# Optimization experiments

Hardware: AMD Instinct MI355X
Metric: run time of the kernel (lower is better)

## Reference

```python
import jax, jax.numpy as jnp
import numpy as np
import math


def _conv1x1(x, w, b):
    # x: [B,C,H,W], w: [O,C], b: [O] -> [B,O,H,W]
    return jnp.einsum('oc,bchw->bohw', w, x) + b[None, :, None, None]


def _attn_branch(x, f_w, f_b, g_w, g_b, h_w, h_b, gamma):
    B, C, H, W = x.shape
    N = H * W
    k_dim = C // 8
    f = _conv1x1(x, f_w, f_b).reshape(B, k_dim, N)  # [B,k,N]
    g = _conv1x1(x, g_w, g_b).reshape(B, k_dim, N)  # [B,k,N]
    # attention[b, n, m] = sum_k f[b,k,n] * g[b,k,m] / sqrt(k_dim)
    scores = jnp.einsum('bkn,bkm->bnm', f, g) / math.sqrt(k_dim)
    attn = jax.nn.softmax(scores, axis=2)  # softmax over last dim (dim=2)
    h = _conv1x1(x, h_w, h_b).reshape(B, C, N)  # [B,C,N]
    sa_map = jnp.einsum('bcn,bnm->bcm', h, attn).reshape(B, C, H, W)
    return gamma[0] * sa_map + x


def setup_inputs() -> dict:
    key = jax.random.key(0)
    ks = jax.random.split(key, 8)
    B, C, H, W = 4, 256, 64, 64
    kd = C // 8
    scale_in = 1.0 / math.sqrt(C)
    return {
        'x1': jax.random.normal(ks[0], (B, C, H, W), jnp.float32),
        'x2': jax.random.normal(ks[1], (B, C, H, W), jnp.float32),
        'f_w': jax.random.normal(ks[2], (kd, C), jnp.float32) * scale_in,
        'f_b': jnp.zeros((kd,), jnp.float32),
        'g_w': jax.random.normal(ks[3], (kd, C), jnp.float32) * scale_in,
        'g_b': jnp.zeros((kd,), jnp.float32),
        'h1_w': jax.random.normal(ks[4], (C, C), jnp.float32) * scale_in,
        'h1_b': jnp.zeros((C,), jnp.float32),
        'h2_w': jax.random.normal(ks[5], (C, C), jnp.float32) * scale_in,
        'h2_b': jnp.zeros((C,), jnp.float32),
        'gamma1': jax.random.normal(ks[6], (1,), jnp.float32),
        'gamma2': jax.random.normal(ks[7], (1,), jnp.float32),
    }


def reference(x1, x2, f_w, f_b, g_w, g_b, h1_w, h1_b, h2_w, h2_b, gamma1, gamma2):
    y1 = _attn_branch(x1, f_w, f_b, g_w, g_b, h1_w, h1_b, gamma1)
    y2 = _attn_branch(x2, f_w, f_b, g_w, g_b, h2_w, h2_b, gamma2)
    return (y1, y2)
```

## Files before the change

### kernel.cpp

```cpp
#include <hip/hip_runtime.h>
#include <hip/hip_bf16.h>
#include <math.h>

#define NDIM 4096
#define CDIM 256
#define KD   32
#define SCALE 0.17677669529663687f
#define SHIFT 8.0f

typedef __attribute__((ext_vector_type(8))) short short8;
typedef __attribute__((ext_vector_type(4))) float f32x4;
typedef unsigned short u16;
typedef unsigned int u32;

__device__ __forceinline__ u32 f2bf(float x) {
  union { float f; u32 u; } v; v.f = x;
  return (v.u + 0x7FFFu + ((v.u >> 16) & 1u)) >> 16;
}

__device__ __forceinline__ u32 pack_bf16x2(float a, float b) {
  __hip_bfloat162 h2 = __float22bfloat162_rn(make_float2(a, b));
  u32 r;
  __builtin_memcpy(&r, &h2, 4);
  return r;
}

#define MFMA16(a, b, c) __builtin_amdgcn_mfma_f32_16x16x32_bf16((a), (b), (c), 0, 0, 0)

__global__ void cast_all_kernel(const float* __restrict__ h1w,
                                const float* __restrict__ h2w,
                                const float* __restrict__ fw,
                                const float* __restrict__ gw,
                                u16* __restrict__ dst) {
  int i = blockIdx.x * 256 + threadIdx.x;
  float v;
  if (i < 65536) v = h1w[i];
  else if (i < 131072) v = h2w[i - 65536];
  else if (i < 139264) v = fw[i - 131072];
  else v = gw[i - 139264];
  dst[i] = (u16)f2bf(v);
}

__global__ __launch_bounds__(256) void transpose_cast_kernel(
    const float* __restrict__ x1, const float* __restrict__ x2,
    u16* __restrict__ xt) {
  __shared__ float ts[64][68];
  const int t = threadIdx.x;
  const int ntile = blockIdx.x * 64, Ctile = blockIdx.y * 64, z = blockIdx.z;
  const float* xb = ((z >> 2) ? x2 : x1) + (size_t)(z & 3) * CDIM * NDIM;
  u16* xtb = xt + (size_t)z * NDIM * CDIM;
  const int r = t >> 4, c4 = (t & 15) * 4;
#pragma unroll
  for (int i = 0; i < 4; i++) {
    float4 v = *(const float4*)&xb[(size_t)(Ctile + r + i * 16) * NDIM + ntile + c4];
    *(float4*)&ts[r + i * 16][c4] = v;
  }
  __syncthreads();
  const int n = t >> 2, Cg = (t & 3) * 16;
  u32 pk[8];
#pragma unroll
  for (int j = 0; j < 8; j++) {
    u32 lo = f2bf(ts[Cg + 2 * j][n]);
    u32 hi = f2bf(ts[Cg + 2 * j + 1][n]);
    pk[j] = lo | (hi << 16);
  }
  uint4* dst = (uint4*)&xtb[(size_t)(ntile + n) * CDIM + Ctile + Cg];
  dst[0] = make_uint4(pk[0], pk[1], pk[2], pk[3]);
  dst[1] = make_uint4(pk[4], pk[5], pk[6], pk[7]);
}

__global__ __launch_bounds__(256) void conv_fg_kernel(
    const u16* __restrict__ Wf, const float* __restrict__ fbias,
    const u16* __restrict__ Wg, const float* __restrict__ gbias,
    const u16* __restrict__ xt, u16* __restrict__ ftT, u16* __restrict__ gtT) {
  const int t = threadIdx.x, w = t >> 6, l = t & 63, li = l & 15, q = l >> 4;
  const int ntile = blockIdx.x * 64, bb = blockIdx.y;
  const u16* xtb = xt + (size_t)bb * NDIM * CDIM;
  f32x4 zero4 = {0.f, 0.f, 0.f, 0.f};
  f32x4 acc[2][2];
  for (int i = 0; i < 2; i++) for (int j = 0; j < 2; j++) acc[i][j] = zero4;
  const int nrow = ntile + w * 16 + li;

  for (int k0 = 0; k0 < CDIM; k0 += 32) {
    short8 bx = *(const short8*)&xtb[(size_t)nrow * CDIM + k0 + q * 8];
    short8 af0 = *(const short8*)&Wf[(size_t)(li) * CDIM + k0 + q * 8];
    short8 af1 = *(const short8*)&Wf[(size_t)(16 + li) * CDIM + k0 + q * 8];
    short8 ag0 = *(const short8*)&Wg[(size_t)(li) * CDIM + k0 + q * 8];
    short8 ag1 = *(const short8*)&Wg[(size_t)(16 + li) * CDIM + k0 + q * 8];
    acc[0][0] = MFMA16(af0, bx, acc[0][0]);
    acc[0][1] = MFMA16(af1, bx, acc[0][1]);
    acc[1][0] = MFMA16(ag0, bx, acc[1][0]);
    acc[1][1] = MFMA16(ag1, bx, acc[1][1]);
  }
  u16* outs[2] = {ftT + (size_t)bb * NDIM * KD, gtT + (size_t)bb * NDIM * KD};
  const float* biases[2] = {fbias, gbias};
#pragma unroll
  for (int fg = 0; fg < 2; fg++) {
#pragma unroll
    for (int os = 0; os < 2; os++) {
      float b0 = biases[fg][os * 16 + q * 4 + 0];
      float b1 = biases[fg][os * 16 + q * 4 + 1];
      float b2 = biases[fg][os * 16 + q * 4 + 2];
      float b3 = biases[fg][os * 16 + q * 4 + 3];
      u32 p0 = f2bf(acc[fg][os][0] + b0) | (f2bf(acc[fg][os][1] + b1) << 16);
      u32 p1 = f2bf(acc[fg][os][2] + b2) | (f2bf(acc[fg][os][3] + b3) << 16);
      *(uint2*)&outs[fg][(size_t)nrow * KD + os * 16 + q * 4] = make_uint2(p0, p1);
    }
  }
}

__global__ __launch_bounds__(256) void stats_kernel(
    const u16* __restrict__ ft, const u16* __restrict__ gt,
    float* __restrict__ L) {
  __shared__ float zred[32][64];
  const int t = threadIdx.x, w = t >> 6, l = t & 63, li = l & 15, q = l >> 4;
  const int n0 = blockIdx.x * 32;
  const int bb = blockIdx.z * 4 + blockIdx.y;
  const u16* ftb = ft + (size_t)bb * NDIM * KD;
  const u16* gtb = gt + (size_t)bb * NDIM * KD;
  f32x4 zero4 = {0.f, 0.f, 0.f, 0.f};

  short8 a0 = *(const short8*)&ftb[(size_t)(n0 + li) * KD + q * 8];
  short8 a1 = *(const short8*)&ftb[(size_t)(n0 + 16 + li) * KD + q * 8];
  f32x4 z0 = zero4, z1 = zero4;

#pragma unroll 2
  for (int it = 0; it < 64; it++) {
    int m = (it * 4 + w) * 16;
    short8 bf = *(const short8*)&gtb[(size_t)(m + li) * KD + q * 8];
    f32x4 S0 = MFMA16(a0, bf, zero4);
    f32x4 S1 = MFMA16(a1, bf, zero4);
#pragma unroll
    for (int reg = 0; reg < 4; reg++) {
      z0[reg] += __expf(S0[reg] * SCALE - SHIFT);
      z1[reg] += __expf(S1[reg] * SCALE - SHIFT);
    }
  }
#pragma unroll
  for (int reg = 0; reg < 4; reg++) {
    zred[q * 4 + reg][w * 16 + li] = z0[reg];
    zred[16 + q * 4 + reg][w * 16 + li] = z1[reg];
  }
  __syncthreads();
  const int r = t >> 3, i8 = t & 7;
  float4 s1 = *(const float4*)&zred[r][i8 * 8];
  float4 s2 = *(const float4*)&zred[r][i8 * 8 + 4];
  float sum = s1.x + s1.y + s1.z + s1.w + s2.x + s2.y + s2.z + s2.w;
  sum += __shfl_xor(sum, 1, 8);
  sum += __shfl_xor(sum, 2, 8);
  sum += __shfl_xor(sum, 4, 8);
  if (i8 == 0) L[(size_t)bb * NDIM + n0 + r] = SHIFT + __logf(sum);
}

__global__ __launch_bounds__(256) void conv_h_kernel(
    const u16* __restrict__ Wall, const float* __restrict__ b1,
    const float* __restrict__ b2, const u16* __restrict__ xt,
    const float* __restrict__ L, u16* __restrict__ outH) {
  const int t = threadIdx.x, w = t >> 6, l = t & 63, li = l & 15, q = l >> 4;
  const int ntile = blockIdx.x * 64;
  const int o0 = blockIdx.y * 64 + w * 16;
  const int bb = blockIdx.z, branch = bb >> 2;
  const u16* W = Wall + (size_t)branch * CDIM * CDIM;
  const float* bias = branch ? b2 : b1;
  const u16* xtb = xt + (size_t)bb * NDIM * CDIM;
  const float* Lb = L + (size_t)bb * NDIM;
  u16* ob = outH + (size_t)bb * CDIM * NDIM;
  f32x4 zero4 = {0.f, 0.f, 0.f, 0.f};
  f32x4 acc[4];
  for (int i = 0; i < 4; i++) acc[i] = zero4;

  for (int k0 = 0; k0 < CDIM; k0 += 32) {
    short8 a = *(const short8*)&W[(size_t)(o0 + li) * CDIM + k0 + q * 8];
#pragma unroll
    for (int ns = 0; ns < 4; ns++) {
      short8 bf = *(const short8*)&xtb[(size_t)(ntile + ns * 16 + li) * CDIM + k0 + q * 8];
      acc[ns] = MFMA16(a, bf, acc[ns]);
    }
  }
  float bv[4];
#pragma unroll
  for (int reg = 0; reg < 4; reg++) bv[reg] = bias[o0 + q * 4 + reg];
#pragma unroll
  for (int ns = 0; ns < 4; ns++) {
    int n = ntile + ns * 16 + li;
    float ex = __expf(-Lb[n]);
#pragma unroll
    for (int reg = 0; reg < 4; reg++) {
      int c = o0 + q * 4 + reg;
      ob[(size_t)c * NDIM + n] = (u16)f2bf((acc[ns][reg] + bv[reg]) * ex);
    }
  }
}

__global__ __launch_bounds__(1024, 4) void apply_kernel(
    const u16* __restrict__ ft, const u16* __restrict__ gt,
    const u16* __restrict__ h,
    const float* __restrict__ x1, const float* __restrict__ x2,
    const float* __restrict__ gamma1, const float* __restrict__ gamma2,
    float* __restrict__ out) {
  __shared__ u16 Pt[2][128][132];
  const int t = threadIdx.x, w = t >> 6, l = t & 63, li = l & 15, q = l >> 4;
  const int bid = blockIdx.x;
  const int bb = bid & 7;
  const int mtile = (bid >> 3) * 128;
  const int br = bb >> 2, b = bb & 3;
  const u16* ftb = ft + (size_t)bb * NDIM * KD;
  const u16* gtb = gt + (size_t)bb * NDIM * KD;
  const u16* hb = h + (size_t)bb * CDIM * NDIM;
  const float* xb = (br ? x2 : x1) + (size_t)b * CDIM * NDIM;
  const float gmv = br ? gamma2[0] : gamma1[0];
  float* ob = out + (size_t)bb * CDIM * NDIM;

  const int msub_s = w >> 1, npair = w & 1;
  const int c0 = (w & 7) * 32;
  const int mg = (w >> 3) * 64;
  f32x4 zero4 = {0.f, 0.f, 0.f, 0.f};
  short8 gfrag = *(const short8*)&gtb[(size_t)(mtile + msub_s * 16 + li) * KD + q * 8];

  f32x4 acc[2][4];
  for (int i = 0; i < 2; i++) for (int j = 0; j < 4; j++) acc[i][j] = zero4;

  u32 Ppk[4][2];
  short8 afA[4];

#pragma unroll
  for (int j = 0; j < 4; j++) {
    int n = npair * 64 + j * 16;
    short8 a = *(const short8*)&ftb[(size_t)(n + li) * KD + q * 8];
    f32x4 S = MFMA16(a, gfrag, zero4);
    Ppk[j][0] = pack_bf16x2(__expf(S[0] * SCALE), __expf(S[1] * SCALE));
    Ppk[j][1] = pack_bf16x2(__expf(S[2] * SCALE), __expf(S[3] * SCALE));
  }
#pragma unroll
  for (int j = 0; j < 4; j++)
    afA[j] = *(const short8*)&ftb[(size_t)(128 + npair * 64 + j * 16 + li) * KD + q * 8];

  for (int i = 0; i < 32; i++) {
    const int n0 = i * 128;
    const int buf = i & 1;
    short8 ah[2][4];
#pragma unroll
    for (int cs = 0; cs < 2; cs++)
#pragma unroll
      for (int kh = 0; kh < 4; kh++)
        ah[cs][kh] = *(const short8*)
            &hb[(size_t)(c0 + cs * 16 + li) * NDIM + n0 + kh * 32 + q * 8];

#pragma unroll
    for (int j = 0; j < 4; j++)
      *(uint2*)&Pt[buf][msub_s * 16 + li][npair * 64 + j * 16 + q * 4] =
          make_uint2(Ppk[j][0], Ppk[j][1]);

#pragma unroll
    for (int j = 0; j < 4; j++) {
      f32x4 S = MFMA16(afA[j], gfrag, zero4);
      Ppk[j][0] = pack_bf16x2(__expf(S[0] * SCALE), __expf(S[1] * SCALE));
      Ppk[j][1] = pack_bf16x2(__expf(S[2] * SCALE), __expf(S[3] * SCALE));
    }

    asm volatile("s_waitcnt lgkmcnt(0)" ::: "memory");
    __builtin_amdgcn_s_barrier();

    {
      int ch2 = (i + 2 < 32) ? i + 2 : 31;
#pragma unroll
      for (int j = 0; j < 4; j++)
        afA[j] = *(const short8*)
            &ftb[(size_t)(ch2 * 128 + npair * 64 + j * 16 + li) * KD + q * 8];
    }

#pragma unroll
    for (int kh = 0; kh < 4; kh++) {
#pragma unroll
      for (int ms = 0; ms < 4; ms++) {
        short8 bm = *(const short8*)&Pt[buf][mg + ms * 16 + li][kh * 32 + q * 8];
        acc[0][ms] = MFMA16(ah[0][kh], bm, acc[0][ms]);
        acc[1][ms] = MFMA16(ah[1][kh], bm, acc[1][ms]);
      }
    }
  }

#pragma unroll
  for (int cs = 0; cs < 2; cs++) {
#pragma unroll
    for (int ms = 0; ms < 4; ms++) {
#pragma unroll
      for (int reg = 0; reg < 4; reg++) {
        int c = c0 + cs * 16 + q * 4 + reg;
        int m = mtile + mg + ms * 16 + li;
        size_t idx = (size_t)c * NDIM + m;
        ob[idx] = gmv * acc[cs][ms][reg] + xb[idx];
      }
    }
  }
}

extern "C" void kernel_launch(void* const* d_in, const int* in_sizes, int n_in,
                              void* d_out, int out_size, void* d_ws, size_t ws_size,
                              hipStream_t stream) {
  const float* x1 = (const float*)d_in[0];
  const float* x2 = (const float*)d_in[1];
  const float* f_w = (const float*)d_in[2];
  const float* f_b = (const float*)d_in[3];
  const float* g_w = (const float*)d_in[4];
  const float* g_b = (const float*)d_in[5];
  const float* h1_w = (const float*)d_in[6];
  const float* h1_b = (const float*)d_in[7];
  const float* h2_w = (const float*)d_in[8];
  const float* h2_b = (const float*)d_in[9];
  const float* gamma1 = (const float*)d_in[10];
  const float* gamma2 = (const float*)d_in[11];
  float* out = (float*)d_out;

  char* ws = (char*)d_ws;
  u16* xt  = (u16*)(ws);
  u16* wh  = (u16*)(ws + 16777216);
  u16* ftw = (u16*)(ws + 33554432);
  u16* gtw = (u16*)(ws + 35651584);
  u16* wWh = (u16*)(ws + 37748736);
  u16* wWf = (u16*)(ws + 38010880);
  u16* wWg = (u16*)(ws + 38027264);
  float* Lw = (float*)(ws + 38043648);

  cast_all_kernel<<<576, 256, 0, stream>>>(h1_w, h2_w, f_w, g_w, wWh);

  transpose_cast_kernel<<<dim3(64, 4, 8), 256, 0, stream>>>(x1, x2, xt);

  conv_fg_kernel<<<dim3(64, 8), 256, 0, stream>>>(wWf, f_b, wWg, g_b, xt, ftw, gtw);

  stats_kernel<<<dim3(128, 4, 2), 256, 0, stream>>>(ftw, gtw, Lw);

  conv_h_kernel<<<dim3(64, 4, 8), 256, 0, stream>>>(wWh, h1_b, h2_b, xt, Lw, wh);

  apply_kernel<<<256, 1024, 0, stream>>>(ftw, gtw, wh, x1, x2,
                                         gamma1, gamma2, out);
}
```

Before: 336.8 us.

## Split attention kernel into producer/consumer warp-specialized wavefronts

Even wavefronts now compute the softmax numerator tile (f·g MFMA plus exp) into a double-buffered LDS tile, and odd wavefronts consume the previous tile with h in a PV MFMA loop. The consumer raises its scheduling priority, and its h loads are double-buffered per k-chunk. The consumer operands are swapped so the epilogue can write float4 vectorized output. The aim is to overlap the exp/score work with the matmul, at the cost of half the waves doing MFMA accumulation and more accumulator registers per consumer wave.

```diff
diff --git a/kernel.cpp b/kernel.cpp
--- a/kernel.cpp
+++ b/kernel.cpp
@@ -211,85 +211,83 @@
   const float gmv = br ? gamma2[0] : gamma1[0];
   float* ob = out + (size_t)bb * CDIM * NDIM;
 
-  const int msub_s = w >> 1, npair = w & 1;
-  const int c0 = (w & 7) * 32;
-  const int mg = (w >> 3) * 64;
+  const bool producer = (w & 1) == 0;
+  const int pidx = w >> 1;
+  const int c0 = (w >> 1) * 32;
   f32x4 zero4 = {0.f, 0.f, 0.f, 0.f};
-  short8 gfrag = *(const short8*)&gtb[(size_t)(mtile + msub_s * 16 + li) * KD + q * 8];
-
-  f32x4 acc[2][4];
-  for (int i = 0; i < 2; i++) for (int j = 0; j < 4; j++) acc[i][j] = zero4;
-
-  u32 Ppk[4][2];
-  short8 afA[4];
-
-#pragma unroll
-  for (int j = 0; j < 4; j++) {
-    int n = npair * 64 + j * 16;
-    short8 a = *(const short8*)&ftb[(size_t)(n + li) * KD + q * 8];
-    f32x4 S = MFMA16(a, gfrag, zero4);
-    Ppk[j][0] = pack_bf16x2(__expf(S[0] * SCALE), __expf(S[1] * SCALE));
-    Ppk[j][1] = pack_bf16x2(__expf(S[2] * SCALE), __expf(S[3] * SCALE));
-  }
-#pragma unroll
-  for (int j = 0; j < 4; j++)
-    afA[j] = *(const short8*)&ftb[(size_t)(128 + npair * 64 + j * 16 + li) * KD + q * 8];
-
-  for (int i = 0; i < 32; i++) {
-    const int n0 = i * 128;
-    const int buf = i & 1;
-    short8 ah[2][4];
-#pragma unroll
-    for (int cs = 0; cs < 2; cs++)
-#pragma unroll
-      for (int kh = 0; kh < 4; kh++)
-        ah[cs][kh] = *(const short8*)
-            &hb[(size_t)(c0 + cs * 16 + li) * NDIM + n0 + kh * 32 + q * 8];
-
-#pragma unroll
-    for (int j = 0; j < 4; j++)
-      *(uint2*)&Pt[buf][msub_s * 16 + li][npair * 64 + j * 16 + q * 4] =
-          make_uint2(Ppk[j][0], Ppk[j][1]);
-
-#pragma unroll
-    for (int j = 0; j < 4; j++) {
-      f32x4 S = MFMA16(afA[j], gfrag, zero4);
-      Ppk[j][0] = pack_bf16x2(__expf(S[0] * SCALE), __expf(S[1] * SCALE));
-      Ppk[j][1] = pack_bf16x2(__expf(S[2] * SCALE), __expf(S[3] * SCALE));
-    }
-
+
+  short8 gfrag;
+  if (producer)
+    gfrag = *(const short8*)&gtb[(size_t)(mtile + pidx * 16 + li) * KD + q * 8];
+
+  f32x4 acc[8][2];
+#pragma unroll
+  for (int i = 0; i < 8; i++)
+#pragma unroll
+    for (int j = 0; j < 2; j++) acc[i][j] = zero4;
+
+  for (int i = 0; i <= 32; i++) {
+    if (producer) {
+      if (i < 32) {
+        const int n0 = i * 128, buf = i & 1;
+        short8 af[8];
+#pragma unroll
+        for (int j = 0; j < 8; j++)
+          af[j] = *(const short8*)&ftb[(size_t)(n0 + j * 16 + li) * KD + q * 8];
+#pragma unroll
+        for (int j = 0; j < 8; j++) {
+          f32x4 S = MFMA16(af[j], gfrag, zero4);
+          u32 p0 = pack_bf16x2(__expf(S[0] * SCALE), __expf(S[1] * SCALE));
+          u32 p1 = pack_bf16x2(__expf(S[2] * SCALE), __expf(S[3] * SCALE));
+          *(uint2*)&Pt[buf][pidx * 16 + li][j * 16 + q * 4] = make_uint2(p0, p1);
+        }
+      }
+    } else {
+      if (i >= 1) {
+        const int n0 = (i - 1) * 128, buf = (i - 1) & 1;
+        short8 ah[2][2];
+#pragma unroll
+        for (int cs = 0; cs < 2; cs++)
+          ah[0][cs] = *(const short8*)
+              &hb[(size_t)(c0 + cs * 16 + li) * NDIM + n0 + q * 8];
+        __builtin_amdgcn_s_setprio(1);
+#pragma unroll
+        for (int kh = 0; kh < 4; kh++) {
+          if (kh < 3) {
+#pragma unroll
+            for (int cs = 0; cs < 2; cs++)
+              ah[(kh + 1) & 1][cs] = *(const short8*)
+                  &hb[(size_t)(c0 + cs * 16 + li) * NDIM + n0 + (kh + 1) * 32 + q * 8];
+          }
+#pragma unroll
+          for (int ms = 0; ms < 8; ms++) {
+            short8 bm = *(const short8*)&Pt[buf][ms * 16 + li][kh * 32 + q * 8];
+            acc[ms][0] = MFMA16(bm, ah[kh & 1][0], acc[ms][0]);
+            acc[ms][1] = MFMA16(bm, ah[kh & 1][1], acc[ms][1]);
+          }
+        }
+        __builtin_amdgcn_s_setprio(0);
+      }
+    }
     asm volatile("s_waitcnt lgkmcnt(0)" ::: "memory");
     __builtin_amdgcn_s_barrier();
-
-    {
-      int ch2 = (i + 2 < 32) ? i + 2 : 31;
-#pragma unroll
-      for (int j = 0; j < 4; j++)
-        afA[j] = *(const short8*)
-            &ftb[(size_t)(ch2 * 128 + npair * 64 + j * 16 + li) * KD + q * 8];
-    }
-
-#pragma unroll
-    for (int kh = 0; kh < 4; kh++) {
-#pragma unroll
-      for (int ms = 0; ms < 4; ms++) {
-        short8 bm = *(const short8*)&Pt[buf][mg + ms * 16 + li][kh * 32 + q * 8];
-        acc[0][ms] = MFMA16(ah[0][kh], bm, acc[0][ms]);
-        acc[1][ms] = MFMA16(ah[1][kh], bm, acc[1][ms]);
-      }
-    }
-  }
-
-#pragma unroll
-  for (int cs = 0; cs < 2; cs++) {
-#pragma unroll
-    for (int ms = 0; ms < 4; ms++) {
-#pragma unroll
-      for (int reg = 0; reg < 4; reg++) {
-        int c = c0 + cs * 16 + q * 4 + reg;
-        int m = mtile + mg + ms * 16 + li;
+  }
+
+  if (!producer) {
+#pragma unroll
+    for (int ms = 0; ms < 8; ms++) {
+#pragma unroll
+      for (int cs = 0; cs < 2; cs++) {
+        int c = c0 + cs * 16 + li;
+        int m = mtile + ms * 16 + q * 4;
         size_t idx = (size_t)c * NDIM + m;
-        ob[idx] = gmv * acc[cs][ms][reg] + xb[idx];
+        float4 xv = *(const float4*)&xb[idx];
+        float4 o;
+        o.x = gmv * acc[ms][cs][0] + xv.x;
+        o.y = gmv * acc[ms][cs][1] + xv.y;
+        o.z = gmv * acc[ms][cs][2] + xv.z;
+        o.w = gmv * acc[ms][cs][3] + xv.w;
+        *(float4*)&ob[idx] = o;
       }
     }
   }
```

New measurement: 306.9 us. 8.9% less time.
